# Optimization experiments

Hardware: AMD Instinct MI355X
Metric: run time of the kernel (lower is better)

## Reference

```python
import jax, jax.numpy as jnp
import numpy as np

B, T, V, H = 16, 256, 64, 256  # batch, time, num_inputs, hidden_dim
EPS = 1e-5

def _layernorm(h, g, b):
    mu = jnp.mean(h, axis=-1, keepdims=True)
    var = jnp.mean(jnp.square(h - mu), axis=-1, keepdims=True)
    return (h - mu) * jax.lax.rsqrt(var + EPS) * g + b

def setup_inputs() -> dict:
    key = jax.random.key(0)
    ks = jax.random.split(key, 16)
    s1, sH = 1.0, 1.0 / np.sqrt(H)
    sV = 1.0 / np.sqrt(V)
    inp = {
        "x": jax.random.normal(ks[0], (B, T, V), jnp.float32),
        # per-variable GRN params (input_dim=1), stacked over V
        "W1": jax.random.normal(ks[1], (V, H), jnp.float32) * s1,
        "b1": jnp.zeros((V, H), jnp.float32),
        "W2": jax.random.normal(ks[2], (V, H, H), jnp.float32) * sH,
        "b2": jnp.zeros((V, H), jnp.float32),
        "Wg": jax.random.normal(ks[3], (V, H), jnp.float32) * s1,  # first H rows of gate Linear(1,2H)
        "bg": jnp.zeros((V, H), jnp.float32),
        "Ws": jax.random.normal(ks[4], (V, H), jnp.float32) * s1,  # skip_proj Linear(1,H)
        "bs": jnp.zeros((V, H), jnp.float32),
        "g1": jnp.ones((V, H), jnp.float32),
        "be1": jnp.zeros((V, H), jnp.float32),
        # weight network GRN: V -> V, skip is Identity
        "nW1": jax.random.normal(ks[5], (V, V), jnp.float32) * sV,
        "nb1": jnp.zeros((V,), jnp.float32),
        "nW2": jax.random.normal(ks[6], (V, V), jnp.float32) * sV,
        "nb2": jnp.zeros((V,), jnp.float32),
        "nWg": jax.random.normal(ks[7], (V, V), jnp.float32) * sV,  # first V cols of gate Linear(V,2V)
        "nbg": jnp.zeros((V,), jnp.float32),
        "ng": jnp.ones((V,), jnp.float32),
        "nbe": jnp.zeros((V,), jnp.float32),
    }
    return inp

def reference(x, W1, b1, W2, b2, Wg, bg, Ws, bs, g1, be1,
              nW1, nb1, nW2, nb2, nWg, nbg, ng, nbe):
    # --- per-variable GRNs, vectorized over V (input is a scalar per variable) ---
    feat = x[..., None]                                     # [B,T,V,1]
    h1 = feat * W1 + b1                                     # [B,T,V,H]  fc1(1->H)
    res = jnp.einsum('btvh,vhk->btvk', jax.nn.elu(h1), W2) + b2  # fc2(H->H)
    gate = jax.nn.sigmoid(feat * Wg + bg)                   # gate(1->2H)[:H]
    skip = feat * Ws + bs                                   # skip_proj(1->H)
    var_out = _layernorm(skip + gate * res, g1, be1)        # [B,T,V,H]
    # --- weight network GRN on flattened input (V -> V, skip=Identity) ---
    wres = jnp.einsum('btv,vk->btk', jax.nn.elu(x @ nW1 + nb1), nW2) + nb2
    wgate = jax.nn.sigmoid(x @ nWg + nbg)
    wout = _layernorm(x + wgate * wres, ng, nbe)            # [B,T,V]
    weights = jax.nn.softmax(wout, axis=-1)                 # [B,T,V]
    combined = jnp.einsum('btvh,btv->bth', var_out, weights)  # [B,T,H]
    return combined
```

## Files before the change

### kernel.cpp

```cpp
#include <hip/hip_runtime.h>
#include <hip/hip_bf16.h>
#include <stdint.h>

#define NTOK 4096
#define NV 64
#define NH 256
#define LN_EPS 1e-5f

typedef __attribute__((ext_vector_type(8))) short short8;
typedef __attribute__((ext_vector_type(4))) float f32x4;
typedef __attribute__((ext_vector_type(4))) uint32_t u32x4;

__device__ __forceinline__ unsigned short f32_to_bf16(float f) {
    uint32_t u = __builtin_bit_cast(uint32_t, f);
    return (unsigned short)((u + 0x7FFFu + ((u >> 16) & 1u)) >> 16);
}
__device__ __forceinline__ float fsigmoid(float z) { return 1.0f / (1.0f + __expf(-z)); }
__device__ __forceinline__ float felu(float z) { return z > 0.0f ? z : (__expf(z) - 1.0f); }
__device__ __forceinline__ uint32_t pack_bf16x2(float ze, float zo) {
    const uint32_t ue = __builtin_bit_cast(uint32_t, ze) + 0x8000u;
    const uint32_t uo = __builtin_bit_cast(uint32_t, zo) + 0x8000u;
    return __builtin_amdgcn_perm(uo, ue, 0x07060302u);
}
__device__ __forceinline__ void gload16(const void* g, void* l) {
    __builtin_amdgcn_global_load_lds(
        (const __attribute__((address_space(1))) uint32_t*)g,
        (__attribute__((address_space(3))) uint32_t*)l, 16, 0, 0);
}

__global__ __launch_bounds__(256) void k_w2t(const float* __restrict__ W2,
                                             unsigned short* __restrict__ W2T) {
    __shared__ float tile[32][33];
    const int v  = blockIdx.x >> 6;
    const int t  = blockIdx.x & 63;
    const int h0 = (t & 7) * 32;
    const int o0 = (t >> 3) * 32;
    const int r  = threadIdx.x >> 3;
    const int c4 = (threadIdx.x & 7) * 4;
    const float4 d = *(const float4*)(W2 + ((size_t)v * NH + h0 + r) * NH + o0 + c4);
    tile[r][c4 + 0] = d.x; tile[r][c4 + 1] = d.y;
    tile[r][c4 + 2] = d.z; tile[r][c4 + 3] = d.w;
    __syncthreads();
    ushort4 o;
    o.x = f32_to_bf16(tile[c4 + 0][r]);
    o.y = f32_to_bf16(tile[c4 + 1][r]);
    o.z = f32_to_bf16(tile[c4 + 2][r]);
    o.w = f32_to_bf16(tile[c4 + 3][r]);
    *(ushort4*)(W2T + ((size_t)v * NH + o0 + r) * NH + h0 + c4) = o;
}

__global__ __launch_bounds__(256) void k_weights(
    const float* __restrict__ x,
    const float* __restrict__ nW1, const float* __restrict__ nb1,
    const float* __restrict__ nW2, const float* __restrict__ nb2,
    const float* __restrict__ nWg, const float* __restrict__ nbg,
    const float* __restrict__ ng,  const float* __restrict__ nbe,
    float* __restrict__ wout_buf) {
    const int wv = threadIdx.x >> 6;
    const int lane = threadIdx.x & 63;
    const int tok = blockIdx.x * 4 + wv;
    const float xv = x[(size_t)tok * NV + lane];
    float acc1 = nb1[lane], accg = nbg[lane];
#pragma unroll 8
    for (int k = 0; k < 64; ++k) {
        const float xk = __shfl(xv, k);
        acc1 = fmaf(xk, nW1[k * 64 + lane], acc1);
        accg = fmaf(xk, nWg[k * 64 + lane], accg);
    }
    const float h  = felu(acc1);
    const float wg = fsigmoid(accg);
    float acc2 = nb2[lane];
#pragma unroll 8
    for (int k = 0; k < 64; ++k) {
        const float hk = __shfl(h, k);
        acc2 = fmaf(hk, nW2[k * 64 + lane], acc2);
    }
    const float pre = xv + wg * acc2;
    float s = pre;
#pragma unroll
    for (int m = 32; m >= 1; m >>= 1) s += __shfl_xor(s, m);
    const float mu = s * (1.0f / 64.0f);
    const float dd = pre - mu;
    float s2 = dd * dd;
#pragma unroll
    for (int m = 32; m >= 1; m >>= 1) s2 += __shfl_xor(s2, m);
    const float inv = rsqrtf(s2 * (1.0f / 64.0f) + LN_EPS);
    const float wln = dd * inv * ng[lane] + nbe[lane];
    float mx = wln;
#pragma unroll
    for (int m = 32; m >= 1; m >>= 1) mx = fmaxf(mx, __shfl_xor(mx, m));
    const float e = __expf(wln - mx);
    float se = e;
#pragma unroll
    for (int m = 32; m >= 1; m >>= 1) se += __shfl_xor(se, m);
    wout_buf[(size_t)tok * NV + lane] = e / se;
}

__global__ __launch_bounds__(512, 2) void k_main(
    const float* __restrict__ x, const unsigned short* __restrict__ W2T,
    const float* __restrict__ W1, const float* __restrict__ b1,
    const float* __restrict__ Wg, const float* __restrict__ bg,
    const float* __restrict__ Ws, const float* __restrict__ bs,
    const float* __restrict__ b2, const float* __restrict__ g1,
    const float* __restrict__ be1, const float* __restrict__ wgts,
    float* __restrict__ partials,
    float* __restrict__ outacc) {
    __shared__ u32x4 sB[2][1024];
    __shared__ float sRB[2][9][256];
    __shared__ float sX[128][9];
    __shared__ float sW[128][9];
    __shared__ float sLN[128][2][2];

    const int tid  = threadIdx.x;
    const int wid  = tid >> 6, lane = tid & 63;
    const int c    = lane & 15, kg = lane >> 4;
    const int tg   = wid >> 1, hh = wid & 1;
    const int bid  = blockIdx.x;
    const int vg   = bid & 7, tt = bid >> 3;
    const int t0   = tt * 128, vbase = vg * 8;

    const unsigned short* W2Tv0 = W2T + (size_t)vbase * (NH * NH);
#pragma unroll
    for (int q = 0; q < 2; ++q) {
        const int idx = wid * 128 + q * 64 + lane;
        const int o = idx >> 2, sl = idx & 3;
        const int s = (sl - (o >> 1)) & 3;
        gload16(W2Tv0 + (size_t)o * NH + s * 8, (char*)sB[0] + (size_t)(wid * 128 + q * 64) * 16);
    }
    {
        const float* rp = wid == 0 ? W1 : wid == 1 ? b1 : wid == 2 ? Wg : wid == 3 ? bg
                        : wid == 4 ? Ws : wid == 5 ? bs : wid == 6 ? b2 : g1;
        gload16(rp + (size_t)vbase * NH + lane * 4, (char*)sRB[0] + wid * 1024);
        if (wid == 0)
            gload16(be1 + (size_t)vbase * NH + lane * 4, (char*)sRB[0] + 8 * 1024);
    }
    for (int e = tid; e < 1024; e += 512) {
        const int row = e >> 3, cc = e & 7;
        sX[row][cc] = x[(size_t)(t0 + row) * NV + vbase + cc];
        sW[row][cc] = wgts[(size_t)(t0 + row) * NV + vbase + cc];
    }
    __syncthreads();

    const int rdbase = hh * 8192 + c * 64 + (((kg + (c >> 1)) & 3) << 4);
    const f32x4 fzero = {0.f, 0.f, 0.f, 0.f};

    f32x4 wacc[2][8];
#pragma unroll
    for (int rt = 0; rt < 2; ++rt)
#pragma unroll
        for (int f = 0; f < 8; ++f) wacc[rt][f] = fzero;

    for (int vi = 0; vi < 8; ++vi) {
        const int rcur = vi & 1;
        const unsigned short* W2Tv = W2T + (size_t)(vbase + vi) * (NH * NH);

        f32x4 acc[2][8];
#pragma unroll
        for (int rt = 0; rt < 2; ++rt)
#pragma unroll
            for (int f = 0; f < 8; ++f) acc[rt][f] = fzero;

        for (int ks = 0; ks < 8; ++ks) {
            const int cb = ks & 1;
            if (ks == 0 && vi < 7) {
                const float* rp = wid == 0 ? W1 : wid == 1 ? b1 : wid == 2 ? Wg : wid == 3 ? bg
                                : wid == 4 ? Ws : wid == 5 ? bs : wid == 6 ? b2 : g1;
                gload16(rp + (size_t)(vbase + vi + 1) * NH + lane * 4,
                        (char*)sRB[rcur ^ 1] + wid * 1024);
                if (wid == 0)
                    gload16(be1 + (size_t)(vbase + vi + 1) * NH + lane * 4,
                            (char*)sRB[rcur ^ 1] + 8 * 1024);
            }
            if (ks < 7 || vi < 7) {
                const unsigned short* Wsrc = (ks < 7) ? W2Tv : (W2Tv + NH * NH);
                const int ksn = (ks < 7) ? (ks + 1) : 0;
#pragma unroll
                for (int q = 0; q < 2; ++q) {
                    const int idx = wid * 128 + q * 64 + lane;
                    const int o = idx >> 2, sl = idx & 3;
                    const int s = (sl - (o >> 1)) & 3;
                    gload16(Wsrc + (size_t)o * NH + ksn * 32 + s * 8,
                            (char*)sB[cb ^ 1] + (size_t)(wid * 128 + q * 64) * 16);
                }
            }
            const int k0 = ks * 32 + kg * 8;
            const float4 wA = *(const float4*)&sRB[rcur][0][k0];
            const float4 wB = *(const float4*)&sRB[rcur][0][k0 + 4];
            const float4 bA = *(const float4*)&sRB[rcur][1][k0];
            const float4 bB = *(const float4*)&sRB[rcur][1][k0 + 4];
            const float xv0 = sX[tg * 32 + c][vi];
            const float xv1 = sX[tg * 32 + 16 + c][vi];
            u32x4 ap0, ap1;
            {
                const float z0 = fmaf(xv0, wA.x, bA.x), z1 = fmaf(xv0, wA.y, bA.y);
                const float z2 = fmaf(xv0, wA.z, bA.z), z3 = fmaf(xv0, wA.w, bA.w);
                const float z4 = fmaf(xv0, wB.x, bB.x), z5 = fmaf(xv0, wB.y, bB.y);
                const float z6 = fmaf(xv0, wB.z, bB.z), z7 = fmaf(xv0, wB.w, bB.w);
                ap0[0] = pack_bf16x2(felu(z0), felu(z1));
                ap0[1] = pack_bf16x2(felu(z2), felu(z3));
                ap0[2] = pack_bf16x2(felu(z4), felu(z5));
                ap0[3] = pack_bf16x2(felu(z6), felu(z7));
            }
            {
                const float z0 = fmaf(xv1, wA.x, bA.x), z1 = fmaf(xv1, wA.y, bA.y);
                const float z2 = fmaf(xv1, wA.z, bA.z), z3 = fmaf(xv1, wA.w, bA.w);
                const float z4 = fmaf(xv1, wB.x, bB.x), z5 = fmaf(xv1, wB.y, bB.y);
                const float z6 = fmaf(xv1, wB.z, bB.z), z7 = fmaf(xv1, wB.w, bB.w);
                ap1[0] = pack_bf16x2(felu(z0), felu(z1));
                ap1[1] = pack_bf16x2(felu(z2), felu(z3));
                ap1[2] = pack_bf16x2(felu(z4), felu(z5));
                ap1[3] = pack_bf16x2(felu(z6), felu(z7));
            }
            const short8 af0 = __builtin_bit_cast(short8, ap0);
            const short8 af1 = __builtin_bit_cast(short8, ap1);
            const char* bb = (const char*)sB[cb] + rdbase;
#pragma unroll
            for (int f = 0; f < 8; ++f) {
                const short8 bf = __builtin_bit_cast(short8, *(const u32x4*)(bb + (f << 10)));
                acc[0][f] = __builtin_amdgcn_mfma_f32_16x16x32_bf16(af0, bf, acc[0][f], 0, 0, 0);
                acc[1][f] = __builtin_amdgcn_mfma_f32_16x16x32_bf16(af1, bf, acc[1][f], 0, 0, 0);
            }
            __syncthreads();
        }

        float xr[2][4], wv_[2][4], gv[8], bev[8];
#pragma unroll
        for (int rt = 0; rt < 2; ++rt)
#pragma unroll
            for (int r = 0; r < 4; ++r) {
                const int tl = tg * 32 + rt * 16 + kg * 4 + r;
                xr[rt][r]  = sX[tl][vi];
                wv_[rt][r] = sW[tl][vi];
            }
        float ps[2][4] = {}, pq[2][4] = {};
#pragma unroll
        for (int f = 0; f < 8; ++f) {
            const int h = ((hh << 3) + f) * 16 + c;
            const float Wg_ = sRB[rcur][2][h], bg_ = sRB[rcur][3][h];
            const float Ws_ = sRB[rcur][4][h], bs_ = sRB[rcur][5][h];
            const float b2_ = sRB[rcur][6][h];
            gv[f] = sRB[rcur][7][h]; bev[f] = sRB[rcur][8][h];
#pragma unroll
            for (int rt = 0; rt < 2; ++rt)
#pragma unroll
                for (int r = 0; r < 4; ++r) {
                    const float y = fmaf(xr[rt][r], Ws_, bs_) +
                                    fsigmoid(fmaf(xr[rt][r], Wg_, bg_)) * (acc[rt][f][r] + b2_);
                    acc[rt][f][r] = y;
                    ps[rt][r] += y;
                    pq[rt][r] = fmaf(y, y, pq[rt][r]);
                }
        }
#pragma unroll
        for (int m = 1; m <= 8; m <<= 1)
#pragma unroll
            for (int rt = 0; rt < 2; ++rt)
#pragma unroll
                for (int r = 0; r < 4; ++r) {
                    ps[rt][r] += __shfl_xor(ps[rt][r], m);
                    pq[rt][r] += __shfl_xor(pq[rt][r], m);
                }
        if (c == 0) {
#pragma unroll
            for (int rt = 0; rt < 2; ++rt)
#pragma unroll
                for (int r = 0; r < 4; ++r) {
                    const int tl = tg * 32 + rt * 16 + kg * 4 + r;
                    *(float2*)&sLN[tl][hh][0] = float2{ps[rt][r], pq[rt][r]};
                }
        }
        __syncthreads();
#pragma unroll
        for (int rt = 0; rt < 2; ++rt)
#pragma unroll
            for (int r = 0; r < 4; ++r) {
                const int tl = tg * 32 + rt * 16 + kg * 4 + r;
                const float4 q4 = *(const float4*)&sLN[tl][0][0];
                const float mu = (q4.x + q4.z) * (1.0f / 256.0f);
                const float vr = (q4.y + q4.w) * (1.0f / 256.0f) - mu * mu;
                const float iv = rsqrtf(vr + LN_EPS);
#pragma unroll
                for (int f = 0; f < 8; ++f)
                    wacc[rt][f][r] = fmaf(wv_[rt][r],
                                          fmaf((acc[rt][f][r] - mu) * iv, gv[f], bev[f]),
                                          wacc[rt][f][r]);
            }
    }

    if (partials) {
        float* P = partials + (size_t)vg * NTOK * NH;
#pragma unroll
        for (int rt = 0; rt < 2; ++rt)
#pragma unroll
            for (int r = 0; r < 4; ++r) {
                float* rowp = P + (size_t)(t0 + tg * 32 + rt * 16 + kg * 4 + r) * NH + hh * 128 + c;
#pragma unroll
                for (int f = 0; f < 8; ++f) rowp[f * 16] = wacc[rt][f][r];
            }
    } else {
#pragma unroll
        for (int rt = 0; rt < 2; ++rt)
#pragma unroll
            for (int r = 0; r < 4; ++r) {
                float* rowp = outacc + (size_t)(t0 + tg * 32 + rt * 16 + kg * 4 + r) * NH + hh * 128 + c;
#pragma unroll
                for (int f = 0; f < 8; ++f) atomicAdd(&rowp[f * 16], wacc[rt][f][r]);
            }
    }
}

__global__ __launch_bounds__(256) void k_reduce(const float* __restrict__ P,
                                                float* __restrict__ out) {
    const size_t i = ((size_t)blockIdx.x * 256 + threadIdx.x);
    const f32x4* P4 = (const f32x4*)P;
    f32x4 s = P4[i];
#pragma unroll
    for (int sl = 1; sl < 8; ++sl) s += P4[(size_t)sl * (NTOK * NH / 4) + i];
    ((f32x4*)out)[i] = s;
}

extern "C" void kernel_launch(void* const* d_in, const int* in_sizes, int n_in,
                              void* d_out, int out_size, void* d_ws, size_t ws_size,
                              hipStream_t stream) {
    const float* x   = (const float*)d_in[0];
    const float* W1  = (const float*)d_in[1];
    const float* b1  = (const float*)d_in[2];
    const float* W2  = (const float*)d_in[3];
    const float* b2  = (const float*)d_in[4];
    const float* Wg  = (const float*)d_in[5];
    const float* bg  = (const float*)d_in[6];
    const float* Ws  = (const float*)d_in[7];
    const float* bs  = (const float*)d_in[8];
    const float* g1  = (const float*)d_in[9];
    const float* be1 = (const float*)d_in[10];
    const float* nW1 = (const float*)d_in[11];
    const float* nb1 = (const float*)d_in[12];
    const float* nW2 = (const float*)d_in[13];
    const float* nb2 = (const float*)d_in[14];
    const float* nWg = (const float*)d_in[15];
    const float* nbg = (const float*)d_in[16];
    const float* ng  = (const float*)d_in[17];
    const float* nbe = (const float*)d_in[18];
    float* out = (float*)d_out;

    char* ws = (char*)d_ws;
    float* ws_wgt = (float*)ws;
    unsigned short* ws_W2T = (unsigned short*)(ws + (1 << 20));
    const size_t part_off = (size_t)9 << 20;
    const size_t part_bytes = (size_t)8 * NTOK * NH * 4;
    const bool use_part = ws_size >= part_off + part_bytes;
    float* ws_part = use_part ? (float*)(ws + part_off) : nullptr;

    k_w2t<<<dim3(64 * 64), dim3(256), 0, stream>>>(W2, ws_W2T);
    k_weights<<<dim3(NTOK / 4), dim3(256), 0, stream>>>(x, nW1, nb1, nW2, nb2,
                                                        nWg, nbg, ng, nbe, ws_wgt);
    if (!use_part) hipMemsetAsync(d_out, 0, (size_t)out_size * 4, stream);
    k_main<<<dim3(256), dim3(512), 0, stream>>>(x, ws_W2T, W1, b1, Wg, bg, Ws, bs,
                                                b2, g1, be1, ws_wgt, ws_part, out);
    if (use_part)
        k_reduce<<<dim3(NTOK * NH / 4 / 256), dim3(256), 0, stream>>>(ws_part, out);
}
```

Measured before the change: 141.9 us.

## Halve k_main token tile to 64 rows, doubling grid, add MFMA priority hints

Shrinks the per-block token tile from 128 to 64 and the block from 512 to 256 threads, launching 512 blocks instead of 256, so more CUs get work on a 256-CU part. Each wave now loads twice the W2 tile and parameter rows, the x lookups are hoisted out of the k-loop, and the loops are marked unroll 1. It also raises wave priority around the MFMA block via s_setprio. In exchange, every W2 slice is now streamed by twice as many blocks, which doubles the weight traffic from L2.

Result: slower. 152.4 us (+7.4%).

```diff
diff --git a/kernel.cpp b/kernel.cpp
--- a/kernel.cpp
+++ b/kernel.cpp
@@ -96,7 +96,19 @@
     wout_buf[(size_t)tok * NV + lane] = e / se;
 }
 
-__global__ __launch_bounds__(512, 2) void k_main(
+__device__ __forceinline__ const float* row_ptr(int r, const float* W1, const float* b1,
+                                                const float* Wg, const float* bg,
+                                                const float* Ws, const float* bs,
+                                                const float* b2, const float* g1,
+                                                const float* be1) {
+    switch (r) {
+        case 0: return W1; case 1: return b1; case 2: return Wg; case 3: return bg;
+        case 4: return Ws; case 5: return bs; case 6: return b2; case 7: return g1;
+        default: return be1;
+    }
+}
+
+__global__ __launch_bounds__(256, 2) void k_main(
     const float* __restrict__ x, const unsigned short* __restrict__ W2T,
     const float* __restrict__ W1, const float* __restrict__ b1,
     const float* __restrict__ Wg, const float* __restrict__ bg,
@@ -107,9 +119,9 @@
     float* __restrict__ outacc) {
     __shared__ u32x4 sB[2][1024];
     __shared__ float sRB[2][9][256];
-    __shared__ float sX[128][9];
-    __shared__ float sW[128][9];
-    __shared__ float sLN[128][2][2];
+    __shared__ float sX[64][9];
+    __shared__ float sW[64][9];
+    __shared__ float sLN[64][2][2];
 
     const int tid  = threadIdx.x;
     const int wid  = tid >> 6, lane = tid & 63;
@@ -117,25 +129,28 @@
     const int tg   = wid >> 1, hh = wid & 1;
     const int bid  = blockIdx.x;
     const int vg   = bid & 7, tt = bid >> 3;
-    const int t0   = tt * 128, vbase = vg * 8;
+    const int t0   = tt * 64, vbase = vg * 8;
+
+    const float* r0p = row_ptr(2 * wid,     W1, b1, Wg, bg, Ws, bs, b2, g1, be1);
+    const float* r1p = row_ptr(2 * wid + 1, W1, b1, Wg, bg, Ws, bs, b2, g1, be1);
 
     const unsigned short* W2Tv0 = W2T + (size_t)vbase * (NH * NH);
 #pragma unroll
-    for (int q = 0; q < 2; ++q) {
-        const int idx = wid * 128 + q * 64 + lane;
+    for (int q = 0; q < 4; ++q) {
+        const int idx = wid * 256 + q * 64 + lane;
         const int o = idx >> 2, sl = idx & 3;
         const int s = (sl - (o >> 1)) & 3;
-        gload16(W2Tv0 + (size_t)o * NH + s * 8, (char*)sB[0] + (size_t)(wid * 128 + q * 64) * 16);
-    }
-    {
-        const float* rp = wid == 0 ? W1 : wid == 1 ? b1 : wid == 2 ? Wg : wid == 3 ? bg
-                        : wid == 4 ? Ws : wid == 5 ? bs : wid == 6 ? b2 : g1;
-        gload16(rp + (size_t)vbase * NH + lane * 4, (char*)sRB[0] + wid * 1024);
-        if (wid == 0)
-            gload16(be1 + (size_t)vbase * NH + lane * 4, (char*)sRB[0] + 8 * 1024);
-    }
-    for (int e = tid; e < 1024; e += 512) {
-        const int row = e >> 3, cc = e & 7;
+        gload16(W2Tv0 + (size_t)o * NH + s * 8,
+                (char*)sB[0] + (size_t)(wid * 256 + q * 64) * 16);
+    }
+    gload16(r0p + (size_t)vbase * NH + lane * 4, (char*)sRB[0] + (2 * wid) * 1024);
+    gload16(r1p + (size_t)vbase * NH + lane * 4, (char*)sRB[0] + (2 * wid + 1) * 1024);
+    if (wid == 0)
+        gload16(be1 + (size_t)vbase * NH + lane * 4, (char*)sRB[0] + 8 * 1024);
+#pragma unroll
+    for (int e = 0; e < 2; ++e) {
+        const int ee = tid + e * 256;
+        const int row = ee >> 3, cc = ee & 7;
         sX[row][cc] = x[(size_t)(t0 + row) * NV + vbase + cc];
         sW[row][cc] = wgts[(size_t)(t0 + row) * NV + vbase + cc];
     }
@@ -150,9 +165,12 @@
 #pragma unroll
         for (int f = 0; f < 8; ++f) wacc[rt][f] = fzero;
 
+#pragma unroll 1
     for (int vi = 0; vi < 8; ++vi) {
         const int rcur = vi & 1;
         const unsigned short* W2Tv = W2T + (size_t)(vbase + vi) * (NH * NH);
+        const float xv0 = sX[tg * 32 + c][vi];
+        const float xv1 = sX[tg * 32 + 16 + c][vi];
 
         f32x4 acc[2][8];
 #pragma unroll
@@ -160,13 +178,14 @@
 #pragma unroll
             for (int f = 0; f < 8; ++f) acc[rt][f] = fzero;
 
+#pragma unroll 1
         for (int ks = 0; ks < 8; ++ks) {
             const int cb = ks & 1;
             if (ks == 0 && vi < 7) {
-                const float* rp = wid == 0 ? W1 : wid == 1 ? b1 : wid == 2 ? Wg : wid == 3 ? bg
-                                : wid == 4 ? Ws : wid == 5 ? bs : wid == 6 ? b2 : g1;
-                gload16(rp + (size_t)(vbase + vi + 1) * NH + lane * 4,
-                        (char*)sRB[rcur ^ 1] + wid * 1024);
+                gload16(r0p + (size_t)(vbase + vi + 1) * NH + lane * 4,
+                        (char*)sRB[rcur ^ 1] + (2 * wid) * 1024);
+                gload16(r1p + (size_t)(vbase + vi + 1) * NH + lane * 4,
+                        (char*)sRB[rcur ^ 1] + (2 * wid + 1) * 1024);
                 if (wid == 0)
                     gload16(be1 + (size_t)(vbase + vi + 1) * NH + lane * 4,
                             (char*)sRB[rcur ^ 1] + 8 * 1024);
@@ -175,12 +194,12 @@
                 const unsigned short* Wsrc = (ks < 7) ? W2Tv : (W2Tv + NH * NH);
                 const int ksn = (ks < 7) ? (ks + 1) : 0;
 #pragma unroll
-                for (int q = 0; q < 2; ++q) {
-                    const int idx = wid * 128 + q * 64 + lane;
+                for (int q = 0; q < 4; ++q) {
+                    const int idx = wid * 256 + q * 64 + lane;
                     const int o = idx >> 2, sl = idx & 3;
                     const int s = (sl - (o >> 1)) & 3;
                     gload16(Wsrc + (size_t)o * NH + ksn * 32 + s * 8,
-                            (char*)sB[cb ^ 1] + (size_t)(wid * 128 + q * 64) * 16);
+                            (char*)sB[cb ^ 1] + (size_t)(wid * 256 + q * 64) * 16);
                 }
             }
             const int k0 = ks * 32 + kg * 8;
@@ -188,8 +207,6 @@
             const float4 wB = *(const float4*)&sRB[rcur][0][k0 + 4];
             const float4 bA = *(const float4*)&sRB[rcur][1][k0];
             const float4 bB = *(const float4*)&sRB[rcur][1][k0 + 4];
-            const float xv0 = sX[tg * 32 + c][vi];
-            const float xv1 = sX[tg * 32 + 16 + c][vi];
             u32x4 ap0, ap1;
             {
                 const float z0 = fmaf(xv0, wA.x, bA.x), z1 = fmaf(xv0, wA.y, bA.y);
@@ -214,12 +231,14 @@
             const short8 af0 = __builtin_bit_cast(short8, ap0);
             const short8 af1 = __builtin_bit_cast(short8, ap1);
             const char* bb = (const char*)sB[cb] + rdbase;
+            __builtin_amdgcn_s_setprio(1);
 #pragma unroll
             for (int f = 0; f < 8; ++f) {
                 const short8 bf = __builtin_bit_cast(short8, *(const u32x4*)(bb + (f << 10)));
                 acc[0][f] = __builtin_amdgcn_mfma_f32_16x16x32_bf16(af0, bf, acc[0][f], 0, 0, 0);
                 acc[1][f] = __builtin_amdgcn_mfma_f32_16x16x32_bf16(af1, bf, acc[1][f], 0, 0, 0);
             }
+            __builtin_amdgcn_s_setprio(0);
             __syncthreads();
         }
 
@@ -355,7 +374,7 @@
     k_weights<<<dim3(NTOK / 4), dim3(256), 0, stream>>>(x, nW1, nb1, nW2, nb2,
                                                         nWg, nbg, ng, nbe, ws_wgt);
     if (!use_part) hipMemsetAsync(d_out, 0, (size_t)out_size * 4, stream);
-    k_main<<<dim3(256), dim3(512), 0, stream>>>(x, ws_W2T, W1, b1, Wg, bg, Ws, bs,
+    k_main<<<dim3(512), dim3(256), 0, stream>>>(x, ws_W2T, W1, b1, Wg, bg, Ws, bs,
                                                 b2, g1, be1, ws_wgt, ws_part, out);
     if (use_part)
         k_reduce<<<dim3(NTOK * NH / 4 / 256), dim3(256), 0, stream>>>(ws_part, out);
```
